# Optimization experiments

Hardware: AMD Instinct MI355X
Metric: run time of the kernel (lower is better)

Reference implementation:

```python
import jax, jax.numpy as jnp
import numpy as np

KS = 4          # kernel_size per pseudo-dim (open linear B-splines, degree 1)
GRID = 28       # level-0 grid side
BATCH = 256     # number of graphs
NUM_FIRST_FC = 49


def _grid(n, B):
    """Batched 8-neighborhood grid graph with 2D pseudo-coords in [0,1]."""
    rs, cs = np.meshgrid(np.arange(n), np.arange(n), indexing='ij')
    idx = rs * n + cs
    src_l, dst_l, ps_l = [], [], []
    for dr in (-1, 0, 1):
        for dc in (-1, 0, 1):
            if dr == 0 and dc == 0:
                continue
            r2, c2 = rs + dr, cs + dc
            ok = (r2 >= 0) & (r2 < n) & (c2 >= 0) & (c2 < n)
            src_l.append(idx[ok])
            dst_l.append((r2 * n + c2)[ok])
            m = int(ok.sum())
            ps_l.append(np.stack([np.full(m, (dr + 1) / 2.0),
                                  np.full(m, (dc + 1) / 2.0)], 1))
    src = np.concatenate(src_l)
    dst = np.concatenate(dst_l)
    pseudo = np.concatenate(ps_l).astype(np.float32)
    off = (np.arange(B) * n * n)[:, None]
    src_b = (src[None] + off).reshape(-1)
    dst_b = (dst[None] + off).reshape(-1)
    return (np.stack([src_b, dst_b]).astype(np.int32),
            np.tile(pseudo, (B, 1)))


def _cluster(n, B):
    """Factor-4 (2x2 block) graclus-style cluster assignment, batched."""
    rs, cs = np.meshgrid(np.arange(n), np.arange(n), indexing='ij')
    c = ((rs // 2) * (n // 2) + (cs // 2)).reshape(-1)
    off = (np.arange(B) * (n // 2) ** 2)[:, None]
    return (c[None] + off).reshape(-1).astype(np.int32)


def setup_inputs() -> dict:
    key = jax.random.key(0)
    ks = jax.random.split(key, 16)
    e0, p0 = _grid(GRID, BATCH)          # 28x28 level
    e1, p1 = _grid(GRID // 2, BATCH)     # 14x14 level
    c0 = _cluster(GRID, BATCH)           # 784 -> 196 per graph
    c1 = _cluster(GRID // 2, BATCH)      # 196 -> 49 per graph
    N0 = BATCH * GRID * GRID
    s = 0.1
    inp = {
        'x': jax.random.normal(ks[0], (N0, 1), jnp.float32),
        'edge_index0': jnp.asarray(e0), 'pseudo0': jnp.asarray(p0),
        'edge_index1': jnp.asarray(e1), 'pseudo1': jnp.asarray(p1),
        'cluster0': jnp.asarray(c0), 'cluster1': jnp.asarray(c1),
        'W1': s * jax.random.normal(ks[1], (16, 1, 32), jnp.float32),
        'root1': s * jax.random.normal(ks[2], (1, 32), jnp.float32),
        'b1': jnp.zeros((32,), jnp.float32),
        'W2': s * jax.random.normal(ks[3], (16, 32, 32), jnp.float32),
        'root2': s * jax.random.normal(ks[4], (32, 32), jnp.float32),
        'b2': jnp.zeros((32,), jnp.float32),
        'W3': s * jax.random.normal(ks[5], (16, 32, 64), jnp.float32),
        'root3': s * jax.random.normal(ks[6], (32, 64), jnp.float32),
        'b3': jnp.zeros((64,), jnp.float32),
        'W4': s * jax.random.normal(ks[7], (16, 64, 64), jnp.float32),
        'root4': s * jax.random.normal(ks[8], (64, 64), jnp.float32),
        'b4': jnp.zeros((64,), jnp.float32),
        'fc1_W': s * jax.random.normal(ks[9], (NUM_FIRST_FC * 64, 512), jnp.float32),
        'fc1_b': jnp.zeros((512,), jnp.float32),
        'fc2_W': s * jax.random.normal(ks[10], (512, 10), jnp.float32),
        'fc2_b': jnp.zeros((10,), jnp.float32),
    }
    return inp


def spline_conv(x, src, dst, pseudo, W, root, bias):
    """SplineGCN layer: degree-1 open B-spline weighting over 2D pseudo-coords,
    mean aggregation over incoming edges, plus root weight and bias."""
    n = x.shape[0]
    pos = pseudo * (KS - 1)                       # [E,2] in [0, KS-1]
    i0f = jnp.clip(jnp.floor(pos), 0, KS - 2)
    frac = pos - i0f                              # [E,2]
    i0 = i0f.astype(jnp.int32)
    XW = jnp.einsum('ni,kio->kno', x, W)          # [K, N, out]: per-kernel transform
    msg = jnp.zeros((src.shape[0], W.shape[2]), x.dtype)
    for a in (0, 1):
        wa = frac[:, 0] if a else 1.0 - frac[:, 0]
        for b in (0, 1):
            wb = frac[:, 1] if b else 1.0 - frac[:, 1]
            k = (i0[:, 0] + a) * KS + (i0[:, 1] + b)     # flat kernel index [E]
            msg = msg + (wa * wb)[:, None] * XW[k, src]  # gather per-edge
    agg = jax.ops.segment_sum(msg, dst, num_segments=n)
    deg = jax.ops.segment_sum(jnp.ones_like(dst, dtype=x.dtype), dst,
                              num_segments=n)
    return agg / jnp.maximum(deg, 1.0)[:, None] + x @ root + bias


def pool4(x, cluster):
    # GraclusMaxPool(2): two halving levels == factor-4 cluster max-pool
    return jax.ops.segment_max(x, cluster, num_segments=x.shape[0] // 4)


def reference(x, edge_index0, pseudo0, edge_index1, pseudo1, cluster0, cluster1,
              W1, root1, b1, W2, root2, b2, W3, root3, b3, W4, root4, b4,
              fc1_W, fc1_b, fc2_W, fc2_b):
    s0, d0 = edge_index0[0], edge_index0[1]
    s1, d1 = edge_index1[0], edge_index1[1]
    h = jax.nn.elu(spline_conv(x, s0, d0, pseudo0, W1, root1, b1))
    h = jax.nn.elu(spline_conv(h, s0, d0, pseudo0, W2, root2, b2))
    h = pool4(h, cluster0)
    h = jax.nn.elu(spline_conv(h, s1, d1, pseudo1, W3, root3, b3))
    h = jax.nn.elu(spline_conv(h, s1, d1, pseudo1, W4, root4, b4))
    h = pool4(h, cluster1)
    h = h.reshape(-1, NUM_FIRST_FC * 64)           # [B, 49*64]
    h = jax.nn.elu(h @ fc1_W + fc1_b)
    # dropout is identity in eval / deterministic reference
    logits = h @ fc2_W + fc2_b
    return jax.nn.log_softmax(logits, axis=-1)
```

## Files before the change

### kernel.cpp

```cpp
#include <hip/hip_runtime.h>

typedef unsigned short u16;
typedef short bf16x8 __attribute__((ext_vector_type(8)));
typedef float f32x4 __attribute__((ext_vector_type(4)));

__device__ __constant__ const int DRS[8] = {-1,-1,-1, 0, 0, 1, 1, 1};
__device__ __constant__ const int DCS[8] = {-1, 0, 1,-1, 1,-1, 0, 1};

__device__ inline float bf2f(u16 u) { return __uint_as_float(((unsigned)u) << 16); }
__device__ inline u16 f2bf(float f) {
  unsigned u = __float_as_uint(f);
  return (u16)((u + 0x7fffu + ((u >> 16) & 1u)) >> 16);
}
__device__ inline float eluf(float v) { return v > 0.f ? v : (__expf(v) - 1.f); }

__device__ inline float weff_val(const float* __restrict__ W, int d, int off, int stride) {
  int dd = d >= 4 ? d + 1 : d;
  int dr = dd / 3 - 1, dc = dd - (dd / 3) * 3 - 1;
  int kr0, kr1, nr; float wr0, wr1;
  if (dr < 0)       { kr0 = 0; wr0 = 1.f; kr1 = 0; wr1 = 0.f; nr = 1; }
  else if (dr == 0) { kr0 = 1; wr0 = .5f; kr1 = 2; wr1 = .5f; nr = 2; }
  else              { kr0 = 3; wr0 = 1.f; kr1 = 0; wr1 = 0.f; nr = 1; }
  int kc0, kc1, nc; float wc0, wc1;
  if (dc < 0)       { kc0 = 0; wc0 = 1.f; kc1 = 0; wc1 = 0.f; nc = 1; }
  else if (dc == 0) { kc0 = 1; wc0 = .5f; kc1 = 2; wc1 = .5f; nc = 2; }
  else              { kc0 = 3; wc0 = 1.f; kc1 = 0; wc1 = 0.f; nc = 1; }
  float acc = wr0 * wc0 * W[(kr0 * 4 + kc0) * stride + off];
  if (nc == 2) acc += wr0 * wc1 * W[(kr0 * 4 + kc1) * stride + off];
  if (nr == 2) {
    acc += wr1 * wc0 * W[(kr1 * 4 + kc0) * stride + off];
    if (nc == 2) acc += wr1 * wc1 * W[(kr1 * 4 + kc1) * stride + off];
  }
  return acc;
}

__global__ __launch_bounds__(256) void pack_all(
    const float* __restrict__ W1,
    const float* __restrict__ W2, const float* __restrict__ rt2,
    const float* __restrict__ W3, const float* __restrict__ rt3,
    const float* __restrict__ W4, const float* __restrict__ rt4,
    const float* __restrict__ fcW,
    float* __restrict__ wf1, u16* __restrict__ wp2,
    u16* __restrict__ wp3, u16* __restrict__ wp4, u16* __restrict__ wfc) {
  __shared__ u16 T[32 * 514];
  int blk = blockIdx.x, t = threadIdx.x;
  if (blk < 98) {
    int q = blk;
#pragma unroll
    for (int i = 0; i < 16; ++i) {
      int idx = i * 1024 + t * 4;
      int k = idx >> 9, n = idx & 511;
      float4 v = *reinterpret_cast<const float4*>(fcW + (size_t)(q * 32 + k) * 512 + n);
      T[k * 514 + n]     = f2bf(v.x);
      T[k * 514 + n + 1] = f2bf(v.y);
      T[k * 514 + n + 2] = f2bf(v.z);
      T[k * 514 + n + 3] = f2bf(v.w);
    }
    __syncthreads();
#pragma unroll
    for (int w = 0; w < 8; ++w) {
      int g = w * 256 + t;
      int nt = g >> 6, l = g & 63;
      union { int4 q4; u16 s[8]; } R;
#pragma unroll
      for (int j = 0; j < 8; ++j)
        R.s[j] = T[((l >> 4) * 8 + j) * 514 + nt * 16 + (l & 15)];
      *reinterpret_cast<int4*>(wfc + ((size_t)(q * 32 + nt) * 64 + l) * 8) = R.q4;
    }
    return;
  }
  int idx = (blk - 98) * 256 + t;
  if (idx < 256) {
    int d = idx >> 5, o = idx & 31;
    wf1[idx] = weff_val(W1, d, o, 32);
    return;
  }
  if (idx < 9472) {
    int local = idx - 256;
    int j = local & 7, l = (local >> 3) & 63, chunk = local >> 9;
    int ct = chunk & 1, tap = chunk >> 1;
    int k = (l >> 4) * 8 + j, n = ct * 16 + (l & 15);
    float v = tap < 8 ? weff_val(W2, tap, k * 32 + n, 1024) : rt2[k * 32 + n];
    wp2[local] = f2bf(v);
    return;
  }
  if (idx < 27904) {
    int local = idx - 9472;
    int j = local & 7, l = (local >> 3) & 63, chunk = local >> 9;
    int ct = chunk & 3, tap = chunk >> 2;
    int k = (l >> 4) * 8 + j, n = ct * 16 + (l & 15);
    float v = tap < 8 ? weff_val(W3, tap, k * 64 + n, 2048) : rt3[k * 64 + n];
    wp3[local] = f2bf(v);
    return;
  }
  if (idx < 64768) {
    int local = idx - 27904;
    int j = local & 7, l = (local >> 3) & 63, chunk = local >> 9;
    int q = chunk & 1, tmp = chunk >> 1;
    int ct = tmp & 3, tap = tmp >> 2;
    int k = q * 32 + (l >> 4) * 8 + j, n = ct * 16 + (l & 15);
    float v = tap < 8 ? weff_val(W4, tap, k * 64 + n, 4096) : rt4[k * 64 + n];
    wp4[local] = f2bf(v);
  }
}

__global__ __launch_bounds__(1024) void conv_mega(
    const float* __restrict__ x,
    const float* __restrict__ wf1, const float* __restrict__ rt1, const float* __restrict__ b1,
    const u16* __restrict__ wp2, const float* __restrict__ b2,
    const u16* __restrict__ wp3, const float* __restrict__ b3,
    const u16* __restrict__ wp4, const float* __restrict__ b4,
    u16* __restrict__ A6) {
  extern __shared__ char smem[];
  int4* H1 = (int4*)smem;
  int4* H3 = (int4*)smem;
  u16*  H5 = (u16*)(smem + 17408);
  int4* H4 = (int4*)(smem + 42496);
  u16*  H4u = (u16*)(smem + 42496);
  float* XT = (float*)(smem + 61568);
  int4* H2 = (int4*)(smem + 75520);
  u16*  H2u = (u16*)(smem + 75520);

  int img = blockIdx.x, tid = threadIdx.x;
  int lane = tid & 63, wid = tid >> 6;
  int kcb = lane >> 4, n0 = lane & 15;
  int4 z4 = make_int4(0, 0, 0, 0);

  for (int i = tid; i < 3848; i += 1024) H1[i] = z4;
  if (tid < 960) {
    int r = tid >> 5, c = tid & 31;
    bool in = (r >= 1) && (r <= 28) && (c >= 1) && (c <= 28);
    XT[tid] = in ? x[(size_t)img * 784 + (r - 1) * 28 + (c - 1)] : 0.f;
  }
  __syncthreads();

  if (tid < 784) {
    int px = tid;
    int r = px / 28, c = px - 28 * (px / 28);
    float acc[32];
#pragma unroll
    for (int o = 0; o < 32; ++o) acc[o] = 0.f;
#pragma unroll
    for (int d = 0; d < 8; ++d) {
      float xv = XT[(r + 1 - DRS[d]) * 32 + (c + 1 - DCS[d])];
#pragma unroll
      for (int o = 0; o < 32; ++o) acc[o] = fmaf(xv, wf1[d * 32 + o], acc[o]);
    }
    float inv = 1.f / (float)((3 - (r == 0) - (r == 27)) * (3 - (c == 0) - (c == 27)) - 1);
    float xc = XT[(r + 1) * 32 + c + 1];
    unsigned pk[16];
#pragma unroll
    for (int h = 0; h < 16; ++h) {
      float v0 = eluf(acc[2 * h] * inv + xc * rt1[2 * h] + b1[2 * h]);
      float v1 = eluf(acc[2 * h + 1] * inv + xc * rt1[2 * h + 1] + b1[2 * h + 1]);
      pk[h] = (unsigned)f2bf(v0) | ((unsigned)f2bf(v1) << 16);
    }
#pragma unroll
    for (int kc = 0; kc < 4; ++kc)
      H1[kc * 962 + (r + 1) * 32 + (c + 1)] =
          make_int4(pk[4 * kc], pk[4 * kc + 1], pk[4 * kc + 2], pk[4 * kc + 3]);
  }
  __syncthreads();

  {
    int ctg = wid & 1, t0 = wid >> 1;
    bf16x8 w2[9];
#pragma unroll
    for (int tap = 0; tap < 9; ++tap)
      w2[tap] = *(const bf16x8*)(wp2 + (tap * 2 + ctg) * 512 + lane * 8);
    for (int t = t0; t < 49; t += 8) {
      int pxm = t * 16 + n0;
      int r = pxm / 28, c = pxm - 28 * (pxm / 28);
      f32x4 an = {0,0,0,0}, ar = {0,0,0,0};
#pragma unroll
      for (int d = 0; d < 8; ++d) {
        bf16x8 a = *(const bf16x8*)&H1[kcb * 962 + (r + 1 - DRS[d]) * 32 + (c + 1 - DCS[d])];
        an = __builtin_amdgcn_mfma_f32_16x16x32_bf16(a, w2[d], an, 0, 0, 0);
      }
      {
        bf16x8 a = *(const bf16x8*)&H1[kcb * 962 + (r + 1) * 32 + (c + 1)];
        ar = __builtin_amdgcn_mfma_f32_16x16x32_bf16(a, w2[8], ar, 0, 0, 0);
      }
#pragma unroll
      for (int j = 0; j < 4; ++j) {
        int pm = t * 16 + (lane >> 4) * 4 + j;
        int rm = pm / 28, cm = pm - 28 * (pm / 28);
        float inv = 1.f / (float)((3 - (rm == 0) - (rm == 27)) * (3 - (cm == 0) - (cm == 27)) - 1);
        H2u[pm * 32 + ctg * 16 + n0] = f2bf(eluf(an[j] * inv + ar[j] + b2[ctg * 16 + n0]));
      }
    }
  }
  __syncthreads();

  for (int i = tid; i < 1032; i += 1024) {
    int kc = i / 258, rem = i - 258 * kc;
    int4 v = z4;
    if (rem < 256) {
      int pr = rem >> 4, pc = rem & 15;
      if (pr >= 1 && pr <= 14 && pc >= 1 && pc <= 14) {
        int px0 = (2 * (pr - 1)) * 28 + 2 * (pc - 1);
        union { int4 q; u16 s[8]; } A, B, C, D, R;
        A.q = H2[px0 * 4 + kc]; B.q = H2[(px0 + 1) * 4 + kc];
        C.q = H2[(px0 + 28) * 4 + kc]; D.q = H2[(px0 + 29) * 4 + kc];
#pragma unroll
        for (int e = 0; e < 8; ++e)
          R.s[e] = f2bf(fmaxf(fmaxf(bf2f(A.s[e]), bf2f(B.s[e])),
                              fmaxf(bf2f(C.s[e]), bf2f(D.s[e]))));
        v = R.q;
      }
    }
    H3[i] = v;
  }
  for (int i = tid; i < 2064; i += 1024) H4[i] = z4;
  __syncthreads();

  int ctg = wid & 3, t0 = wid >> 2;
  {
    bf16x8 w3[9];
#pragma unroll
    for (int tap = 0; tap < 9; ++tap)
      w3[tap] = *(const bf16x8*)(wp3 + (tap * 4 + ctg) * 512 + lane * 8);
    for (int t = t0; t < 13; t += 4) {
      int pxm = t * 16 + n0; if (pxm > 195) pxm = 195;
      int r = pxm / 14, c = pxm - 14 * (pxm / 14);
      f32x4 an = {0,0,0,0}, ar = {0,0,0,0};
#pragma unroll
      for (int d = 0; d < 8; ++d) {
        bf16x8 a = *(const bf16x8*)&H3[kcb * 258 + (r + 1 - DRS[d]) * 16 + (c + 1 - DCS[d])];
        an = __builtin_amdgcn_mfma_f32_16x16x32_bf16(a, w3[d], an, 0, 0, 0);
      }
      {
        bf16x8 a = *(const bf16x8*)&H3[kcb * 258 + (r + 1) * 16 + (c + 1)];
        ar = __builtin_amdgcn_mfma_f32_16x16x32_bf16(a, w3[8], ar, 0, 0, 0);
      }
#pragma unroll
      for (int j = 0; j < 4; ++j) {
        int pm = t * 16 + (lane >> 4) * 4 + j;
        if (pm < 196) {
          int rm = pm / 14, cm = pm - 14 * (pm / 14);
          float inv = 1.f / (float)((3 - (rm == 0) - (rm == 13)) * (3 - (cm == 0) - (cm == 13)) - 1);
          int n = ctg * 16 + n0;
          float v = eluf(an[j] * inv + ar[j] + b3[n]);
          H4u[((n >> 3) * 258 + (rm + 1) * 16 + (cm + 1)) * 8 + (n & 7)] = f2bf(v);
        }
      }
    }
  }
  __syncthreads();

  {
    bf16x8 w4[9][2];
#pragma unroll
    for (int tap = 0; tap < 9; ++tap)
#pragma unroll
      for (int q = 0; q < 2; ++q)
        w4[tap][q] = *(const bf16x8*)(wp4 + ((tap * 4 + ctg) * 2 + q) * 512 + lane * 8);
    for (int t = t0; t < 13; t += 4) {
      int pxm = t * 16 + n0; if (pxm > 195) pxm = 195;
      int r = pxm / 14, c = pxm - 14 * (pxm / 14);
      f32x4 an = {0,0,0,0}, ar = {0,0,0,0};
#pragma unroll
      for (int d = 0; d < 8; ++d) {
        int rr = r + 1 - DRS[d], c2 = c + 1 - DCS[d];
#pragma unroll
        for (int q = 0; q < 2; ++q) {
          bf16x8 a = *(const bf16x8*)&H4[(q * 4 + kcb) * 258 + rr * 16 + c2];
          an = __builtin_amdgcn_mfma_f32_16x16x32_bf16(a, w4[d][q], an, 0, 0, 0);
        }
      }
#pragma unroll
      for (int q = 0; q < 2; ++q) {
        bf16x8 a = *(const bf16x8*)&H4[(q * 4 + kcb) * 258 + (r + 1) * 16 + (c + 1)];
        ar = __builtin_amdgcn_mfma_f32_16x16x32_bf16(a, w4[8][q], ar, 0, 0, 0);
      }
#pragma unroll
      for (int j = 0; j < 4; ++j) {
        int pm = t * 16 + (lane >> 4) * 4 + j;
        if (pm < 196) {
          int rm = pm / 14, cm = pm - 14 * (pm / 14);
          float inv = 1.f / (float)((3 - (rm == 0) - (rm == 13)) * (3 - (cm == 0) - (cm == 13)) - 1);
          int n = ctg * 16 + n0;
          H5[pm * 64 + n] = f2bf(eluf(an[j] * inv + ar[j] + b4[n]));
        }
      }
    }
  }
  __syncthreads();

  if (tid < 392) {
    int kc = tid & 7, q = tid >> 3;
    int r2 = q / 7, c2 = q - 7 * (q / 7);
    int px0 = (2 * r2) * 14 + 2 * c2;
    union { int4 q4; u16 s[8]; } A, B, C, D, R;
    A.q4 = *(const int4*)&H5[px0 * 64 + kc * 8];
    B.q4 = *(const int4*)&H5[(px0 + 1) * 64 + kc * 8];
    C.q4 = *(const int4*)&H5[(px0 + 14) * 64 + kc * 8];
    D.q4 = *(const int4*)&H5[(px0 + 15) * 64 + kc * 8];
#pragma unroll
    for (int e = 0; e < 8; ++e)
      R.s[e] = f2bf(fmaxf(fmaxf(bf2f(A.s[e]), bf2f(B.s[e])),
                          fmaxf(bf2f(C.s[e]), bf2f(D.s[e]))));
    *(int4*)(A6 + ((size_t)img * 49 + q) * 64 + kc * 8) = R.q4;
  }
}

__global__ __launch_bounds__(256) void fc1_mfma(
    const u16* __restrict__ A6, const u16* __restrict__ wfc,
    float* __restrict__ part) {
  int blk = blockIdx.x;
  int ks = blk >> 5;
  int rem = blk & 31;
  int mt = rem & 3, nt4 = rem >> 2;
  int lane = threadIdx.x & 63, w = threadIdx.x >> 6;
  int NT = nt4 * 4 + w;
  f32x4 acc[4];
#pragma unroll
  for (int m4 = 0; m4 < 4; ++m4) acc[m4] = {0.f, 0.f, 0.f, 0.f};
  int rbase = mt * 64 + (lane & 15);
  int kb = ks * 224 + (lane >> 4) * 8;
#pragma unroll
  for (int qq = 0; qq < 7; ++qq) {
    bf16x8 bfr = *(const bf16x8*)(wfc + ((size_t)((ks * 7 + qq) * 32 + NT) * 64 + lane) * 8);
#pragma unroll
    for (int m4 = 0; m4 < 4; ++m4) {
      bf16x8 a = *(const bf16x8*)(A6 + (size_t)(rbase + m4 * 16) * 3136 + kb + qq * 32);
      acc[m4] = __builtin_amdgcn_mfma_f32_16x16x32_bf16(a, bfr, acc[m4], 0, 0, 0);
    }
  }
#pragma unroll
  for (int m4 = 0; m4 < 4; ++m4)
#pragma unroll
    for (int j = 0; j < 4; ++j) {
      int row = mt * 64 + m4 * 16 + (lane >> 4) * 4 + j;
      int col = NT * 16 + (lane & 15);
      part[((size_t)ks * 256 + row) * 512 + col] = acc[m4][j];
    }
}

__global__ __launch_bounds__(64) void fc2_kernel(
    const float* __restrict__ part, const float* __restrict__ fc1b,
    const float* __restrict__ W, const float* __restrict__ bias,
    float* __restrict__ out) {
  int bb = blockIdx.x;
  int t = threadIdx.x;
  float acc[10];
#pragma unroll
  for (int o = 0; o < 10; ++o) acc[o] = 0.f;
  for (int k = t; k < 512; k += 64) {
    float s = fc1b[k];
#pragma unroll
    for (int ks = 0; ks < 14; ++ks) s += part[(size_t)ks * 131072 + bb * 512 + k];
    float xv = eluf(s);
#pragma unroll
    for (int o = 0; o < 10; ++o) acc[o] = fmaf(xv, W[k * 10 + o], acc[o]);
  }
#pragma unroll
  for (int o = 0; o < 10; ++o) {
    float v = acc[o];
#pragma unroll
    for (int s = 32; s >= 1; s >>= 1) v += __shfl_xor(v, s);
    acc[o] = v + bias[o];
  }
  float m = acc[0];
#pragma unroll
  for (int o = 1; o < 10; ++o) m = fmaxf(m, acc[o]);
  float sum = 0.f;
#pragma unroll
  for (int o = 0; o < 10; ++o) sum += __expf(acc[o] - m);
  float lse = m + __logf(sum);
  if (t < 10) out[bb * 10 + t] = acc[t] - lse;
}

extern "C" void kernel_launch(void* const* d_in, const int* in_sizes, int n_in,
                              void* d_out, int out_size, void* d_ws, size_t ws_size,
                              hipStream_t stream) {
  const float* x    = (const float*)d_in[0];
  const float* W1   = (const float*)d_in[7];
  const float* r1   = (const float*)d_in[8];
  const float* b1   = (const float*)d_in[9];
  const float* W2   = (const float*)d_in[10];
  const float* r2   = (const float*)d_in[11];
  const float* b2   = (const float*)d_in[12];
  const float* W3   = (const float*)d_in[13];
  const float* r3   = (const float*)d_in[14];
  const float* b3   = (const float*)d_in[15];
  const float* W4   = (const float*)d_in[16];
  const float* r4   = (const float*)d_in[17];
  const float* b4   = (const float*)d_in[18];
  const float* fc1W = (const float*)d_in[19];
  const float* fc1b = (const float*)d_in[20];
  const float* fc2W = (const float*)d_in[21];
  const float* fc2b = (const float*)d_in[22];

  char* wsb = (char*)d_ws;
  float* wf1  = (float*)(wsb + 0);
  u16*   wp2  = (u16*)(wsb + 1024);
  u16*   wp3  = (u16*)(wsb + 19456);
  u16*   wp4  = (u16*)(wsb + 56320);
  u16*   wfc  = (u16*)(wsb + 130048);
  u16*   A6   = (u16*)(wsb + 3341312);
  float* part = (float*)(wsb + 4946944);

  pack_all<<<351, 256, 0, stream>>>(W1, W2, r2, W3, r3, W4, r4, fc1W,
                                    wf1, wp2, wp3, wp4, wfc);

  (void)hipFuncSetAttribute((const void*)conv_mega,
                            hipFuncAttributeMaxDynamicSharedMemorySize, 125696);
  conv_mega<<<256, 1024, 125696, stream>>>(x, wf1, r1, b1, wp2, b2, wp3, b3,
                                           wp4, b4, A6);

  fc1_mfma<<<448, 256, 0, stream>>>(A6, wfc, part);
  fc2_kernel<<<256, 64, 0, stream>>>(part, fc1b, fc2W, fc2b, (float*)d_out);
}
```

Measured before the change: 54.41 us.

## Compute two output-channel tiles per wave and pack bf16 pairs in conv epilogues

Each wave in conv layers 2-4 now computes two 16-wide output-channel tiles for the same pixels, so one A-fragment LDS load feeds two MFMAs. Epilogue stores become packed 32-bit bf16 pairs instead of 16-bit scalars. To keep this consistent, the K (input channel) ordering of the layer 3, layer 4 and fc1 weight packs is permuted so that the interleaved channel pairs in LDS line up with the weights. The cost is more register pressure from doubled weight fragments, plus fewer waves sharing the pixel tiles in layers 3 and 4.

After: 75.17 us. 1.38x slower.

```diff
diff --git a/kernel.cpp b/kernel.cpp
--- a/kernel.cpp
+++ b/kernel.cpp
@@ -13,6 +13,9 @@
   return (u16)((u + 0x7fffu + ((u >> 16) & 1u)) >> 16);
 }
 __device__ inline float eluf(float v) { return v > 0.f ? v : (__expf(v) - 1.f); }
+__device__ inline unsigned pk2(float a, float b) {
+  return (unsigned)f2bf(a) | ((unsigned)f2bf(b) << 16);
+}
 
 __device__ inline float weff_val(const float* __restrict__ W, int d, int off, int stride) {
   int dd = d >= 4 ? d + 1 : d;
@@ -34,6 +37,8 @@
   return acc;
 }
 
+__device__ inline int kperm32(int p) { return (p >> 1) + ((p & 1) << 4); }
+
 __global__ __launch_bounds__(256) void pack_all(
     const float* __restrict__ W1,
     const float* __restrict__ W2, const float* __restrict__ rt2,
@@ -63,8 +68,10 @@
       int nt = g >> 6, l = g & 63;
       union { int4 q4; u16 s[8]; } R;
 #pragma unroll
-      for (int j = 0; j < 8; ++j)
-        R.s[j] = T[((l >> 4) * 8 + j) * 514 + nt * 16 + (l & 15)];
+      for (int j = 0; j < 8; ++j) {
+        int s = (l >> 4) * 8 + j;
+        R.s[j] = T[kperm32(s) * 514 + nt * 16 + (l & 15)];
+      }
       *reinterpret_cast<int4*>(wfc + ((size_t)(q * 32 + nt) * 64 + l) * 8) = R.q4;
     }
     return;
@@ -88,7 +95,7 @@
     int local = idx - 9472;
     int j = local & 7, l = (local >> 3) & 63, chunk = local >> 9;
     int ct = chunk & 3, tap = chunk >> 2;
-    int k = (l >> 4) * 8 + j, n = ct * 16 + (l & 15);
+    int k = kperm32((l >> 4) * 8 + j), n = ct * 16 + (l & 15);
     float v = tap < 8 ? weff_val(W3, tap, k * 64 + n, 2048) : rt3[k * 64 + n];
     wp3[local] = f2bf(v);
     return;
@@ -98,7 +105,7 @@
     int j = local & 7, l = (local >> 3) & 63, chunk = local >> 9;
     int q = chunk & 1, tmp = chunk >> 1;
     int ct = tmp & 3, tap = tmp >> 2;
-    int k = q * 32 + (l >> 4) * 8 + j, n = ct * 16 + (l & 15);
+    int k = q * 32 + kperm32((l >> 4) * 8 + j), n = ct * 16 + (l & 15);
     float v = tap < 8 ? weff_val(W4, tap, k * 64 + n, 4096) : rt4[k * 64 + n];
     wp4[local] = f2bf(v);
   }
@@ -114,17 +121,19 @@
   extern __shared__ char smem[];
   int4* H1 = (int4*)smem;
   int4* H3 = (int4*)smem;
-  u16*  H5 = (u16*)(smem + 17408);
-  int4* H4 = (int4*)(smem + 42496);
-  u16*  H4u = (u16*)(smem + 42496);
+  unsigned* H5u = (unsigned*)(smem + 17408);
+  int4*     H5q = (int4*)(smem + 17408);
+  int4*     H4 = (int4*)(smem + 42496);
+  unsigned* H4u = (unsigned*)(smem + 42496);
   float* XT = (float*)(smem + 61568);
-  int4* H2 = (int4*)(smem + 75520);
-  u16*  H2u = (u16*)(smem + 75520);
+  int4*     H2 = (int4*)(smem + 75520);
+  unsigned* H2u = (unsigned*)(smem + 75520);
 
   int img = blockIdx.x, tid = threadIdx.x;
   int lane = tid & 63, wid = tid >> 6;
   int kcb = lane >> 4, n0 = lane & 15;
   int4 z4 = make_int4(0, 0, 0, 0);
+  f32x4 zz = {0.f, 0.f, 0.f, 0.f};
 
   for (int i = tid; i < 3848; i += 1024) H1[i] = z4;
   if (tid < 960) {
@@ -150,11 +159,9 @@
     float xc = XT[(r + 1) * 32 + c + 1];
     unsigned pk[16];
 #pragma unroll
-    for (int h = 0; h < 16; ++h) {
-      float v0 = eluf(acc[2 * h] * inv + xc * rt1[2 * h] + b1[2 * h]);
-      float v1 = eluf(acc[2 * h + 1] * inv + xc * rt1[2 * h + 1] + b1[2 * h + 1]);
-      pk[h] = (unsigned)f2bf(v0) | ((unsigned)f2bf(v1) << 16);
-    }
+    for (int h = 0; h < 16; ++h)
+      pk[h] = pk2(eluf(acc[2 * h] * inv + xc * rt1[2 * h] + b1[2 * h]),
+                  eluf(acc[2 * h + 1] * inv + xc * rt1[2 * h + 1] + b1[2 * h + 1]));
 #pragma unroll
     for (int kc = 0; kc < 4; ++kc)
       H1[kc * 962 + (r + 1) * 32 + (c + 1)] =
@@ -163,30 +170,34 @@
   __syncthreads();
 
   {
-    int ctg = wid & 1, t0 = wid >> 1;
-    bf16x8 w2[9];
+    bf16x8 w2[9][2];
 #pragma unroll
     for (int tap = 0; tap < 9; ++tap)
-      w2[tap] = *(const bf16x8*)(wp2 + (tap * 2 + ctg) * 512 + lane * 8);
-    for (int t = t0; t < 49; t += 8) {
+#pragma unroll
+      for (int ct = 0; ct < 2; ++ct)
+        w2[tap][ct] = *(const bf16x8*)(wp2 + (tap * 2 + ct) * 512 + lane * 8);
+    for (int t = wid; t < 49; t += 16) {
       int pxm = t * 16 + n0;
       int r = pxm / 28, c = pxm - 28 * (pxm / 28);
-      f32x4 an = {0,0,0,0}, ar = {0,0,0,0};
+      f32x4 an[2] = {zz, zz}, ar[2] = {zz, zz};
 #pragma unroll
       for (int d = 0; d < 8; ++d) {
         bf16x8 a = *(const bf16x8*)&H1[kcb * 962 + (r + 1 - DRS[d]) * 32 + (c + 1 - DCS[d])];
-        an = __builtin_amdgcn_mfma_f32_16x16x32_bf16(a, w2[d], an, 0, 0, 0);
+        an[0] = __builtin_amdgcn_mfma_f32_16x16x32_bf16(a, w2[d][0], an[0], 0, 0, 0);
+        an[1] = __builtin_amdgcn_mfma_f32_16x16x32_bf16(a, w2[d][1], an[1], 0, 0, 0);
       }
       {
         bf16x8 a = *(const bf16x8*)&H1[kcb * 962 + (r + 1) * 32 + (c + 1)];
-        ar = __builtin_amdgcn_mfma_f32_16x16x32_bf16(a, w2[8], ar, 0, 0, 0);
+        ar[0] = __builtin_amdgcn_mfma_f32_16x16x32_bf16(a, w2[8][0], ar[0], 0, 0, 0);
+        ar[1] = __builtin_amdgcn_mfma_f32_16x16x32_bf16(a, w2[8][1], ar[1], 0, 0, 0);
       }
 #pragma unroll
       for (int j = 0; j < 4; ++j) {
         int pm = t * 16 + (lane >> 4) * 4 + j;
         int rm = pm / 28, cm = pm - 28 * (pm / 28);
         float inv = 1.f / (float)((3 - (rm == 0) - (rm == 27)) * (3 - (cm == 0) - (cm == 27)) - 1);
-        H2u[pm * 32 + ctg * 16 + n0] = f2bf(eluf(an[j] * inv + ar[j] + b2[ctg * 16 + n0]));
+        H2u[pm * 16 + n0] = pk2(eluf(an[0][j] * inv + ar[0][j] + b2[n0]),
+                                eluf(an[1][j] * inv + ar[1][j] + b2[16 + n0]));
       }
     }
   }
@@ -214,24 +225,28 @@
   for (int i = tid; i < 2064; i += 1024) H4[i] = z4;
   __syncthreads();
 
-  int ctg = wid & 3, t0 = wid >> 2;
+  int ct0 = wid & 1, t0 = wid >> 1;
   {
-    bf16x8 w3[9];
+    bf16x8 w3[9][2];
 #pragma unroll
     for (int tap = 0; tap < 9; ++tap)
-      w3[tap] = *(const bf16x8*)(wp3 + (tap * 4 + ctg) * 512 + lane * 8);
-    for (int t = t0; t < 13; t += 4) {
+#pragma unroll
+      for (int cc = 0; cc < 2; ++cc)
+        w3[tap][cc] = *(const bf16x8*)(wp3 + (tap * 4 + ct0 * 2 + cc) * 512 + lane * 8);
+    for (int t = t0; t < 13; t += 8) {
       int pxm = t * 16 + n0; if (pxm > 195) pxm = 195;
       int r = pxm / 14, c = pxm - 14 * (pxm / 14);
-      f32x4 an = {0,0,0,0}, ar = {0,0,0,0};
+      f32x4 an[2] = {zz, zz}, ar[2] = {zz, zz};
 #pragma unroll
       for (int d = 0; d < 8; ++d) {
         bf16x8 a = *(const bf16x8*)&H3[kcb * 258 + (r + 1 - DRS[d]) * 16 + (c + 1 - DCS[d])];
-        an = __builtin_amdgcn_mfma_f32_16x16x32_bf16(a, w3[d], an, 0, 0, 0);
+        an[0] = __builtin_amdgcn_mfma_f32_16x16x32_bf16(a, w3[d][0], an[0], 0, 0, 0);
+        an[1] = __builtin_amdgcn_mfma_f32_16x16x32_bf16(a, w3[d][1], an[1], 0, 0, 0);
       }
       {
         bf16x8 a = *(const bf16x8*)&H3[kcb * 258 + (r + 1) * 16 + (c + 1)];
-        ar = __builtin_amdgcn_mfma_f32_16x16x32_bf16(a, w3[8], ar, 0, 0, 0);
+        ar[0] = __builtin_amdgcn_mfma_f32_16x16x32_bf16(a, w3[8][0], ar[0], 0, 0, 0);
+        ar[1] = __builtin_amdgcn_mfma_f32_16x16x32_bf16(a, w3[8][1], ar[1], 0, 0, 0);
       }
 #pragma unroll
       for (int j = 0; j < 4; ++j) {
@@ -239,49 +254,48 @@
         if (pm < 196) {
           int rm = pm / 14, cm = pm - 14 * (pm / 14);
           float inv = 1.f / (float)((3 - (rm == 0) - (rm == 13)) * (3 - (cm == 0) - (cm == 13)) - 1);
-          int n = ctg * 16 + n0;
-          float v = eluf(an[j] * inv + ar[j] + b3[n]);
-          H4u[((n >> 3) * 258 + (rm + 1) * 16 + (cm + 1)) * 8 + (n & 7)] = f2bf(v);
+          unsigned v = pk2(eluf(an[0][j] * inv + ar[0][j] + b3[ct0 * 32 + n0]),
+                           eluf(an[1][j] * inv + ar[1][j] + b3[ct0 * 32 + 16 + n0]));
+          H4u[((ct0 * 4 + (n0 >> 2)) * 258 + (rm + 1) * 16 + (cm + 1)) * 4 + (n0 & 3)] = v;
         }
       }
     }
   }
   __syncthreads();
 
-  {
-    bf16x8 w4[9][2];
-#pragma unroll
-    for (int tap = 0; tap < 9; ++tap)
-#pragma unroll
-      for (int q = 0; q < 2; ++q)
-        w4[tap][q] = *(const bf16x8*)(wp4 + ((tap * 4 + ctg) * 2 + q) * 512 + lane * 8);
-    for (int t = t0; t < 13; t += 4) {
-      int pxm = t * 16 + n0; if (pxm > 195) pxm = 195;
-      int r = pxm / 14, c = pxm - 14 * (pxm / 14);
-      f32x4 an = {0,0,0,0}, ar = {0,0,0,0};
+  for (int t = t0; t < 13; t += 8) {
+    int pxm = t * 16 + n0; if (pxm > 195) pxm = 195;
+    int r = pxm / 14, c = pxm - 14 * (pxm / 14);
+    f32x4 an[2] = {zz, zz}, ar[2] = {zz, zz};
+#pragma unroll
+    for (int kq = 0; kq < 2; ++kq) {
+      bf16x8 w4[9][2];
+#pragma unroll
+      for (int tap = 0; tap < 9; ++tap)
+#pragma unroll
+        for (int cc = 0; cc < 2; ++cc)
+          w4[tap][cc] = *(const bf16x8*)(wp4 + ((tap * 4 + ct0 * 2 + cc) * 2 + kq) * 512 + lane * 8);
 #pragma unroll
       for (int d = 0; d < 8; ++d) {
-        int rr = r + 1 - DRS[d], c2 = c + 1 - DCS[d];
-#pragma unroll
-        for (int q = 0; q < 2; ++q) {
-          bf16x8 a = *(const bf16x8*)&H4[(q * 4 + kcb) * 258 + rr * 16 + c2];
-          an = __builtin_amdgcn_mfma_f32_16x16x32_bf16(a, w4[d][q], an, 0, 0, 0);
-        }
-      }
-#pragma unroll
-      for (int q = 0; q < 2; ++q) {
-        bf16x8 a = *(const bf16x8*)&H4[(q * 4 + kcb) * 258 + (r + 1) * 16 + (c + 1)];
-        ar = __builtin_amdgcn_mfma_f32_16x16x32_bf16(a, w4[8][q], ar, 0, 0, 0);
-      }
-#pragma unroll
-      for (int j = 0; j < 4; ++j) {
-        int pm = t * 16 + (lane >> 4) * 4 + j;
-        if (pm < 196) {
-          int rm = pm / 14, cm = pm - 14 * (pm / 14);
-          float inv = 1.f / (float)((3 - (rm == 0) - (rm == 13)) * (3 - (cm == 0) - (cm == 13)) - 1);
-          int n = ctg * 16 + n0;
-          H5[pm * 64 + n] = f2bf(eluf(an[j] * inv + ar[j] + b4[n]));
-        }
+        bf16x8 a = *(const bf16x8*)&H4[(kq * 4 + kcb) * 258 + (r + 1 - DRS[d]) * 16 + (c + 1 - DCS[d])];
+        an[0] = __builtin_amdgcn_mfma_f32_16x16x32_bf16(a, w4[d][0], an[0], 0, 0, 0);
+        an[1] = __builtin_amdgcn_mfma_f32_16x16x32_bf16(a, w4[d][1], an[1], 0, 0, 0);
+      }
+      {
+        bf16x8 a = *(const bf16x8*)&H4[(kq * 4 + kcb) * 258 + (r + 1) * 16 + (c + 1)];
+        ar[0] = __builtin_amdgcn_mfma_f32_16x16x32_bf16(a, w4[8][0], ar[0], 0, 0, 0);
+        ar[1] = __builtin_amdgcn_mfma_f32_16x16x32_bf16(a, w4[8][1], ar[1], 0, 0, 0);
+      }
+    }
+#pragma unroll
+    for (int j = 0; j < 4; ++j) {
+      int pm = t * 16 + (lane >> 4) * 4 + j;
+      if (pm < 196) {
+        int rm = pm / 14, cm = pm - 14 * (pm / 14);
+        float inv = 1.f / (float)((3 - (rm == 0) - (rm == 13)) * (3 - (cm == 0) - (cm == 13)) - 1);
+        H5u[pm * 32 + ct0 * 16 + n0] =
+            pk2(eluf(an[0][j] * inv + ar[0][j] + b4[ct0 * 32 + n0]),
+                eluf(an[1][j] * inv + ar[1][j] + b4[ct0 * 32 + 16 + n0]));
       }
     }
   }
@@ -292,10 +306,10 @@
     int r2 = q / 7, c2 = q - 7 * (q / 7);
     int px0 = (2 * r2) * 14 + 2 * c2;
     union { int4 q4; u16 s[8]; } A, B, C, D, R;
-    A.q4 = *(const int4*)&H5[px0 * 64 + kc * 8];
-    B.q4 = *(const int4*)&H5[(px0 + 1) * 64 + kc * 8];
-    C.q4 = *(const int4*)&H5[(px0 + 14) * 64 + kc * 8];
-    D.q4 = *(const int4*)&H5[(px0 + 15) * 64 + kc * 8];
+    A.q4 = H5q[px0 * 8 + kc];
+    B.q4 = H5q[(px0 + 1) * 8 + kc];
+    C.q4 = H5q[(px0 + 14) * 8 + kc];
+    D.q4 = H5q[(px0 + 15) * 8 + kc];
 #pragma unroll
     for (int e = 0; e < 8; ++e)
       R.s[e] = f2bf(fmaxf(fmaxf(bf2f(A.s[e]), bf2f(B.s[e])),
```
